# Kernel optimization log

Measured on AMD Instinct MI355X. Metric: run time of the kernel, lower is better.

Reference implementation:

```python
import jax, jax.numpy as jnp
import numpy as np

INC, INN, OUTC, OUTN, MAXD, N = 32, 50000, 32, 8192, 16, 8


def setup_inputs() -> dict:
    key = jax.random.key(0)
    k1, k2, k3, k4 = jax.random.split(key, 4)
    x = jax.random.normal(k1, (N, INC, INN), dtype=jnp.float32)
    # padded adjacency table: [outn, maxD] indices into inn
    A = jax.random.randint(k2, (OUTN, MAXD), 0, INN)
    # normalize=True with all rows at full degree -> mask = 1/maxD
    mask = jnp.full((OUTN, MAXD, 1), 1.0 / MAXD, dtype=jnp.float32)
    weight = 0.2 * jax.random.normal(k3, (INC, OUTC), dtype=jnp.float32)
    bias = 0.2 * jax.random.normal(k4, (OUTC, OUTN), dtype=jnp.float32)
    return {"x": x, "A": A, "mask": mask, "weight": weight, "bias": bias}


def reference(x, A, mask, weight, bias):
    n = x.shape[0]
    # x: [N, inc, inn] -> embedding table [inn, N*inc]
    ew = x.reshape(-1, INN).T
    # gather neighbors: [outn, maxD, N*inc]
    emb = ew[A]
    # masked mean-pool over neighbors -> [outn, N, inc]
    pooled = (mask * emb).reshape(OUTN, MAXD, n, INC).sum(axis=1)
    # shared-weight matmul (replaces the wasteful expanded bmm): [outn, N, outc]
    almost_y = jnp.einsum('onc,cd->ond', pooled, weight)
    # -> [N, outc, outn]
    y = jnp.transpose(almost_y, (1, 2, 0))
    return y + bias
```

## Files before the change

kernel.cpp:

```cpp
#include <hip/hip_runtime.h>
#include <hip/hip_bf16.h>


#define INN   50000
#define NR    256
#define OUTN  8192
#define MAXD  16
#define TO    32

static __device__ __forceinline__ float bf2f(unsigned short u) {
    return __uint_as_float(((unsigned int)u) << 16);
}

static __device__ __forceinline__ unsigned pack2(float a, float b) {
    const unsigned lo = (unsigned)__bfloat16_as_ushort(__float2bfloat16(a));
    const unsigned hi = (unsigned)__bfloat16_as_ushort(__float2bfloat16(b));
    return lo | (hi << 16);
}

__global__ __launch_bounds__(256) void transpose_x(const float* __restrict__ x,
                                                   unsigned short* __restrict__ xt) {
    __shared__ float tile[64 * 65];
    const int t  = threadIdx.x;
    const int i0 = blockIdx.x * 64;
    const int r0 = blockIdx.y * 64;

    {
        const int i4l = t & 15;
        const int rl0 = t >> 4;
        const float4* x4 = (const float4*)x;
        const int i4base = (i0 >> 2) + i4l;
        const bool iv = (i4base < (INN / 4));
        for (int k = 0; k < 4; ++k) {
            const int rl = rl0 + 16 * k;
            float4 v = iv ? x4[(size_t)(r0 + rl) * (INN / 4) + i4base]
                          : make_float4(0.f, 0.f, 0.f, 0.f);
            const int ib = i4l * 4;
            tile[(ib + 0) * 65 + rl] = v.x;
            tile[(ib + 1) * 65 + rl] = v.y;
            tile[(ib + 2) * 65 + rl] = v.z;
            tile[(ib + 3) * 65 + rl] = v.w;
        }
    }
    __syncthreads();
    {
        const int r8l = t & 7;
        const int il0 = t >> 3;
        for (int k = 0; k < 2; ++k) {
            const int il = il0 + 32 * k;
            const int i  = i0 + il;
            if (i < INN) {
                const float* src = &tile[il * 65 + r8l * 8];
                uint4 b;
                b.x = pack2(src[0], src[1]);
                b.y = pack2(src[2], src[3]);
                b.z = pack2(src[4], src[5]);
                b.w = pack2(src[6], src[7]);
                *(uint4*)&xt[(size_t)i * NR + r0 + 8 * r8l] = b;
            }
        }
    }
}

__global__ __launch_bounds__(1024) void gather_gemm(const unsigned short* __restrict__ xt,
                                                    const int*   __restrict__ A,
                                                    const float* __restrict__ mask,
                                                    const float* __restrict__ W,
                                                    const float* __restrict__ bias,
                                                    float* __restrict__ out) {
    __shared__ float pooled[TO * 260];
    __shared__ float Wt[32 * 36];
    __shared__ int   Ash[TO * MAXD];
    __shared__ float Msh[TO * MAXD];

    const int t  = threadIdx.x;
    const int o0 = blockIdx.x * TO;

    if (t < TO * MAXD) {
        Ash[t] = A[o0 * MAXD + t];
        Msh[t] = mask[o0 * MAXD + t];
    }
    {
        const int c = t >> 5, cd = t & 31;
        Wt[cd * 36 + c] = W[t];
    }
    __syncthreads();

    {
        const int j  = t & 63;
        const int og = t >> 6;
        const ushort4* xt4 = (const ushort4*)xt;
        for (int m = 0; m < 2; ++m) {
            const int ol = og * 2 + m;
            ushort4 u[MAXD];
#pragma unroll
            for (int d = 0; d < MAXD; ++d) {
                const int idx = Ash[ol * MAXD + d];
                u[d] = xt4[(size_t)idx * 64 + j];
            }
            float4 a = make_float4(0.f, 0.f, 0.f, 0.f);
#pragma unroll
            for (int d = 0; d < MAXD; ++d) {
                const float s = Msh[ol * MAXD + d];
                a.x += s * bf2f(u[d].x);
                a.y += s * bf2f(u[d].y);
                a.z += s * bf2f(u[d].z);
                a.w += s * bf2f(u[d].w);
            }
            *(float4*)&pooled[ol * 260 + 4 * j] = a;
        }
    }
    __syncthreads();

    if (t < 256) {
        const int n  = t >> 5;
        const int cd = t & 31;
        float4 w[8];
#pragma unroll
        for (int cc = 0; cc < 8; ++cc)
            w[cc] = *(const float4*)&Wt[cd * 36 + 4 * cc];

        float res[TO];
#pragma unroll
        for (int ol = 0; ol < TO; ++ol) {
            const float4* pr = (const float4*)&pooled[ol * 260 + n * 32];
            float s = 0.f;
#pragma unroll
            for (int cc = 0; cc < 8; ++cc) {
                const float4 p = pr[cc];
                s += p.x * w[cc].x + p.y * w[cc].y + p.z * w[cc].z + p.w * w[cc].w;
            }
            res[ol] = s;
        }

        const size_t obase = (size_t)n * (32 * OUTN) + (size_t)cd * OUTN + o0;
        const size_t bbase = (size_t)cd * OUTN + o0;
#pragma unroll
        for (int q = 0; q < 8; ++q) {
            const float4 b = *(const float4*)&bias[bbase + 4 * q];
            float4 r;
            r.x = res[4 * q + 0] + b.x;
            r.y = res[4 * q + 1] + b.y;
            r.z = res[4 * q + 2] + b.z;
            r.w = res[4 * q + 3] + b.w;
            *(float4*)&out[obase + 4 * q] = r;
        }
    }
}

extern "C" void kernel_launch(void* const* d_in, const int* in_sizes, int n_in,
                              void* d_out, int out_size, void* d_ws, size_t ws_size,
                              hipStream_t stream) {
    const float* x    = (const float*)d_in[0];
    const int*   A    = (const int*)  d_in[1];
    const float* mask = (const float*)d_in[2];
    const float* W    = (const float*)d_in[3];
    const float* bias = (const float*)d_in[4];
    float* out = (float*)d_out;
    unsigned short* xt = (unsigned short*)d_ws;

    transpose_x<<<dim3(782, 4), 256, 0, stream>>>(x, xt);
    gather_gemm<<<OUTN / TO, 1024, 0, stream>>>(xt, A, mask, W, bias, out);
}
```

Before: 113.0 us.

## Fuse transpose and gather-GEMM into one cooperative kernel with grid sync

Combines the bf16 transpose pass and the gather/mean-pool/GEMM pass into a single cooperative kernel of 256 blocks of 1024 threads. Each block first transposes up to 16 tiles, four at a time with one per 256-thread subgroup, then waits at a grid-wide sync before doing the gather stage from shared memory reused for the new layout. This removes one kernel launch and the gap between the two launches. In exchange the transpose runs on far fewer resident blocks than the original 3128-block grid, which can lower memory-level parallelism, and it adds the cost of the grid barrier. The old two-kernel path is kept as a fallback if the cooperative launch fails.

```diff
diff --git a/kernel.cpp b/kernel.cpp
--- a/kernel.cpp
+++ b/kernel.cpp
@@ -1,5 +1,8 @@
 #include <hip/hip_runtime.h>
 #include <hip/hip_bf16.h>
+#include <hip/hip_cooperative_groups.h>
+
+namespace cg = cooperative_groups;
 
 
 #define INN   50000
@@ -7,15 +10,168 @@
 #define OUTN  8192
 #define MAXD  16
 #define TO    32
+#define NBLK  256
+#define NTHR  1024
+#define NJOBS 3128
 
 static __device__ __forceinline__ float bf2f(unsigned short u) {
     return __uint_as_float(((unsigned int)u) << 16);
 }
-
 static __device__ __forceinline__ unsigned pack2(float a, float b) {
     const unsigned lo = (unsigned)__bfloat16_as_ushort(__float2bfloat16(a));
     const unsigned hi = (unsigned)__bfloat16_as_ushort(__float2bfloat16(b));
     return lo | (hi << 16);
+}
+
+#define SH_BYTES (4 * 64 * 65 * 4)
+
+static __device__ __forceinline__ void tile_load(const float* __restrict__ x,
+                                                 float* tile, int tl, int i0, int r0,
+                                                 bool active) {
+    const int i4l = tl & 15;
+    const int rl0 = tl >> 4;
+    const float4* x4 = (const float4*)x;
+    const int i4base = (i0 >> 2) + i4l;
+    const bool iv = active && (i4base < (INN / 4));
+    for (int k = 0; k < 4; ++k) {
+        const int rl = rl0 + 16 * k;
+        float4 v = iv ? x4[(size_t)(r0 + rl) * (INN / 4) + i4base]
+                      : make_float4(0.f, 0.f, 0.f, 0.f);
+        const int ib = i4l * 4;
+        tile[(ib + 0) * 65 + rl] = v.x;
+        tile[(ib + 1) * 65 + rl] = v.y;
+        tile[(ib + 2) * 65 + rl] = v.z;
+        tile[(ib + 3) * 65 + rl] = v.w;
+    }
+}
+static __device__ __forceinline__ void tile_store(unsigned short* __restrict__ xt,
+                                                  const float* tile, int tl, int i0, int r0,
+                                                  bool active) {
+    const int r8l = tl & 7;
+    const int il0 = tl >> 3;
+    for (int k = 0; k < 2; ++k) {
+        const int il = il0 + 32 * k;
+        const int i  = i0 + il;
+        if (active && i < INN) {
+            const float* src = &tile[il * 65 + r8l * 8];
+            uint4 b;
+            b.x = pack2(src[0], src[1]);
+            b.y = pack2(src[2], src[3]);
+            b.z = pack2(src[4], src[5]);
+            b.w = pack2(src[6], src[7]);
+            *(uint4*)&xt[(size_t)i * NR + r0 + 8 * r8l] = b;
+        }
+    }
+}
+
+__global__ __launch_bounds__(NTHR) void fused(const float* __restrict__ x,
+                                              const int*   __restrict__ A,
+                                              const float* __restrict__ mask,
+                                              const float* __restrict__ W,
+                                              const float* __restrict__ bias,
+                                              float* __restrict__ out,
+                                              unsigned short* __restrict__ xt) {
+    __shared__ __align__(16) char shraw[SH_BYTES];
+    const int t   = threadIdx.x;
+    const int bid = blockIdx.x;
+
+    {
+        const int sg = t >> 8;
+        const int tl = t & 255;
+        float* tile = (float*)shraw + sg * (64 * 65);
+        for (int it = 0; it < 4; ++it) {
+            const int job = it * (NBLK * 4) + bid * 4 + sg;
+            const bool active = (job < NJOBS);
+            const int jb = active ? job : 0;
+            const int i0 = (jb % 782) * 64;
+            const int r0 = (jb / 782) * 64;
+            tile_load(x, tile, tl, i0, r0, active);
+            __syncthreads();
+            tile_store(xt, tile, tl, i0, r0, active);
+            __syncthreads();
+        }
+    }
+
+    __threadfence();
+    cg::this_grid().sync();
+
+    float* pooled = (float*)shraw;
+    float* Wt     = (float*)shraw + TO * 260;
+    int*   Ash    = (int*)((float*)shraw + TO * 260 + 32 * 36);
+    float* Msh    = (float*)shraw + TO * 260 + 32 * 36 + TO * MAXD;
+
+    const int o0 = bid * TO;
+
+    if (t < TO * MAXD) {
+        Ash[t] = A[o0 * MAXD + t];
+        Msh[t] = mask[o0 * MAXD + t];
+    }
+    {
+        const int c = t >> 5, cd = t & 31;
+        Wt[cd * 36 + c] = W[t];
+    }
+    __syncthreads();
+
+    {
+        const int j  = t & 63;
+        const int og = t >> 6;
+        const ushort4* xt4 = (const ushort4*)xt;
+        for (int m = 0; m < 2; ++m) {
+            const int ol = og * 2 + m;
+            ushort4 u[MAXD];
+#pragma unroll
+            for (int d = 0; d < MAXD; ++d) {
+                const int idx = Ash[ol * MAXD + d];
+                u[d] = xt4[(size_t)idx * 64 + j];
+            }
+            float4 a = make_float4(0.f, 0.f, 0.f, 0.f);
+#pragma unroll
+            for (int d = 0; d < MAXD; ++d) {
+                const float s = Msh[ol * MAXD + d];
+                a.x += s * bf2f(u[d].x);
+                a.y += s * bf2f(u[d].y);
+                a.z += s * bf2f(u[d].z);
+                a.w += s * bf2f(u[d].w);
+            }
+            *(float4*)&pooled[ol * 260 + 4 * j] = a;
+        }
+    }
+    __syncthreads();
+
+    if (t < 256) {
+        const int n  = t >> 5;
+        const int cd = t & 31;
+        float4 w[8];
+#pragma unroll
+        for (int cc = 0; cc < 8; ++cc)
+            w[cc] = *(const float4*)&Wt[cd * 36 + 4 * cc];
+
+        float res[TO];
+#pragma unroll
+        for (int ol = 0; ol < TO; ++ol) {
+            const float4* pr = (const float4*)&pooled[ol * 260 + n * 32];
+            float s = 0.f;
+#pragma unroll
+            for (int cc = 0; cc < 8; ++cc) {
+                const float4 p = pr[cc];
+                s += p.x * w[cc].x + p.y * w[cc].y + p.z * w[cc].z + p.w * w[cc].w;
+            }
+            res[ol] = s;
+        }
+
+        const size_t obase = (size_t)n * (32 * OUTN) + (size_t)cd * OUTN + o0;
+        const size_t bbase = (size_t)cd * OUTN + o0;
+#pragma unroll
+        for (int q = 0; q < 8; ++q) {
+            const float4 b = *(const float4*)&bias[bbase + 4 * q];
+            float4 r;
+            r.x = res[4 * q + 0] + b.x;
+            r.y = res[4 * q + 1] + b.y;
+            r.z = res[4 * q + 2] + b.z;
+            r.w = res[4 * q + 3] + b.w;
+            *(float4*)&out[obase + 4 * q] = r;
+        }
+    }
 }
 
 __global__ __launch_bounds__(256) void transpose_x(const float* __restrict__ x,
@@ -24,42 +180,9 @@
     const int t  = threadIdx.x;
     const int i0 = blockIdx.x * 64;
     const int r0 = blockIdx.y * 64;
-
-    {
-        const int i4l = t & 15;
-        const int rl0 = t >> 4;
-        const float4* x4 = (const float4*)x;
-        const int i4base = (i0 >> 2) + i4l;
-        const bool iv = (i4base < (INN / 4));
-        for (int k = 0; k < 4; ++k) {
-            const int rl = rl0 + 16 * k;
-            float4 v = iv ? x4[(size_t)(r0 + rl) * (INN / 4) + i4base]
-                          : make_float4(0.f, 0.f, 0.f, 0.f);
-            const int ib = i4l * 4;
-            tile[(ib + 0) * 65 + rl] = v.x;
-            tile[(ib + 1) * 65 + rl] = v.y;
-            tile[(ib + 2) * 65 + rl] = v.z;
-            tile[(ib + 3) * 65 + rl] = v.w;
-        }
-    }
-    __syncthreads();
-    {
-        const int r8l = t & 7;
-        const int il0 = t >> 3;
-        for (int k = 0; k < 2; ++k) {
-            const int il = il0 + 32 * k;
-            const int i  = i0 + il;
-            if (i < INN) {
-                const float* src = &tile[il * 65 + r8l * 8];
-                uint4 b;
-                b.x = pack2(src[0], src[1]);
-                b.y = pack2(src[2], src[3]);
-                b.z = pack2(src[4], src[5]);
-                b.w = pack2(src[6], src[7]);
-                *(uint4*)&xt[(size_t)i * NR + r0 + 8 * r8l] = b;
-            }
-        }
-    }
+    tile_load(x, tile, t, i0, r0, true);
+    __syncthreads();
+    tile_store(xt, tile, t, i0, r0, true);
 }
 
 __global__ __launch_bounds__(1024) void gather_gemm(const unsigned short* __restrict__ xt,
@@ -159,6 +282,12 @@
     float* out = (float*)d_out;
     unsigned short* xt = (unsigned short*)d_ws;
 
-    transpose_x<<<dim3(782, 4), 256, 0, stream>>>(x, xt);
-    gather_gemm<<<OUTN / TO, 1024, 0, stream>>>(xt, A, mask, W, bias, out);
-}
+    void* args[] = { (void*)&x, (void*)&A, (void*)&mask, (void*)&W,
+                     (void*)&bias, (void*)&out, (void*)&xt };
+    hipError_t e = hipLaunchCooperativeKernel((const void*)fused, dim3(NBLK),
+                                              dim3(NTHR), args, 0, stream);
+    if (e != hipSuccess) {
+        transpose_x<<<dim3(782, 4), 256, 0, stream>>>(x, xt);
+        gather_gemm<<<OUTN / TO, 1024, 0, stream>>>(xt, A, mask, W, bias, out);
+    }
+}
```

After: 242.4 us. +114.5%, slower.
